# Performance work log

Measured on AMD Instinct MI355X. Metric: run time of the kernel, lower is better.

Reference implementation:

```python
import jax, jax.numpy as jnp
import numpy as np

N_FFT = 4096
HOP = 1024
WIN = 300          # wiener_win_len (frames per independent Wiener chunk)
EPS = 1e-10
SCALE_FACTOR = 10.0


def hann(n):
    # torch.hann_window (periodic)
    return 0.5 * (1.0 - jnp.cos(2.0 * jnp.pi * jnp.arange(n) / n))


def stft(x, window):
    # x: (N, C, T) -> complex (N, C, B, F), center=True, reflect pad, onesided
    pad = N_FFT // 2
    xp = jnp.pad(x, ((0, 0), (0, 0), (pad, pad)), mode='reflect')
    n_frames = 1 + (xp.shape[-1] - N_FFT) // HOP
    idx = jnp.arange(n_frames)[:, None] * HOP + jnp.arange(N_FFT)[None, :]
    frames = xp[..., idx] * window                      # (N,C,F,n_fft)
    spec = jnp.fft.rfft(frames, axis=-1)                # (N,C,F,B)
    return jnp.swapaxes(spec, -1, -2)                   # (N,C,B,F)


def istft(spec, window, length):
    # spec: (..., B, F) complex -> (..., length) real; center=True inverse
    frames = jnp.fft.irfft(jnp.swapaxes(spec, -1, -2), n=N_FFT, axis=-1) * window
    n_frames = frames.shape[-2]
    out_len = N_FFT + HOP * (n_frames - 1)
    idx = jnp.arange(n_frames)[:, None] * HOP + jnp.arange(N_FFT)[None, :]
    out = jnp.zeros(frames.shape[:-2] + (out_len,), frames.dtype).at[..., idx].add(frames)
    wsum = jnp.zeros((out_len,), frames.dtype).at[idx].add(
        jnp.broadcast_to(window ** 2, idx.shape))
    out = out / jnp.where(wsum > 1e-11, wsum, 1.0)
    pad = N_FFT // 2
    return out[..., pad:pad + length]


def wiener_chunk(v, x, niter):
    # openunmix.filtering.wiener (softmask=False, residual=False) on one chunk.
    # v: (T, B, C, S) real target magnitudes; x: (T, B, C) complex mix STFT.
    phase = jnp.exp(1j * jnp.angle(x))                  # mixture phase init
    y = (v * phase[..., None]).astype(jnp.complex64)    # (T,B,C,S)
    max_abs = jnp.maximum(1.0, jnp.max(jnp.abs(x)) / SCALE_FACTOR)
    x = x / max_abs
    y = y / max_abs
    C = x.shape[-1]
    reg = np.sqrt(EPS) * jnp.eye(C, dtype=jnp.complex64)
    for _ in range(niter):  # expectation_maximization, one pass per iter
        psd = jnp.mean(jnp.abs(y) ** 2, axis=2)         # (T,B,S) channel-avg PSD
        # spatial covariance per bin/source, normalized by eps + sum_t psd
        R = jnp.einsum('tbcs,tbds->bcds', y, jnp.conj(y))
        R = R / (EPS + jnp.sum(psd, axis=0))[:, None, None, :]
        Cxx = reg + jnp.einsum('tbs,bcds->tbcd', psd.astype(jnp.complex64), R)
        inv = jnp.linalg.inv(Cxx)                       # (T,B,C,C)
        gain = jnp.einsum('bacs,tbcd->tbads', R, inv) * psd[:, :, None, None, :]
        y = jnp.einsum('tbacs,tbc->tbas', gain, x)      # (T,B,C,S)
    return y * max_abs


def setup_inputs() -> dict:
    key = jax.random.key(0)
    k1, k2 = jax.random.split(key)
    audio = jax.random.normal(k1, (2, 2, 613376), dtype=jnp.float32)
    W = jax.random.normal(k2, (4, 2049), dtype=jnp.float32)  # per-target per-bin mask logits
    return {'audio': audio, 'W': W, 'niter': 1}


def reference(audio, W, niter):
    window = hann(N_FFT).astype(audio.dtype)
    mix = stft(audio, window)                           # (N,C,B,F) complex
    X = jnp.abs(mix)                                    # ComplexNorm power=1
    # target models (stand-in: per-bin sigmoid masks); input detached as in torch
    Xd = jax.lax.stop_gradient(X)
    masks = jax.nn.sigmoid(W)                           # (S,B)
    specs = Xd[..., None] * jnp.transpose(masks)[None, None, :, None, :]  # (N,C,B,F,S)
    v = jnp.transpose(specs, (0, 3, 2, 1, 4))           # (N,F,B,C,S)
    xm = jnp.transpose(mix, (0, 3, 2, 1))               # (N,F,B,C)
    N, F, B, C = xm.shape
    S = v.shape[-1]
    n_chunks = F // WIN
    vc = v.reshape(N, n_chunks, WIN, B, C, S)
    xc = xm.reshape(N, n_chunks, WIN, B, C)
    wfun = lambda vv, xx: wiener_chunk(vv, xx, niter)
    yc = jax.vmap(jax.vmap(wfun))(vc, xc)               # (N,chunks,T,B,C,S)
    y = yc.reshape(N, F, B, C, S)
    y = jnp.transpose(y, (0, 4, 3, 2, 1))               # (N,S,C,B,F)
    estimates = istft(y, window, audio.shape[-1])       # (N,S,C,T)
    return estimates
```

## Files before the change

### kernel.cpp

```cpp
#include <hip/hip_runtime.h>
#include <math.h>

#define TLEN 613376
#define OLEN 617472
#define NFR  600
#define NB   2049
#define PI_F  3.14159265358979323846f
#define PI2_F 6.28318530717958647693f
#define PHYS(i) ((i) + ((i) >> 4))

__device__ __forceinline__ float winf(int j) {
  return 0.5f - 0.5f * __cosf(1.5339807878856412e-3f * (float)j);
}

__device__ __forceinline__ float wsum_at(int m) {
  int f_max = m >> 10; if (f_max > 599) f_max = 599;
  int f_min = (m - 3072) >> 10; if (f_min < 0) f_min = 0;
  float ws = 0.f;
  for (int f2 = f_min; f2 <= f_max; ++f2) {
    float w = winf(m - (f2 << 10));
    ws += w * w;
  }
  return (ws > 1e-11f) ? ws : 1.0f;
}

__device__ __forceinline__ float reflect_load(const float* __restrict__ x, int pos) {
  int k = pos - 2048;
  if (k < 0) k = -k;
  else if (k >= TLEN) k = 2 * TLEN - 2 - k;
  return x[k];
}

__device__ __forceinline__ float2 cmul(float2 a, float2 b) {
  return make_float2(a.x * b.x - a.y * b.y, a.x * b.y + a.y * b.x);
}
__device__ __forceinline__ float2 cadd(float2 a, float2 b) { return make_float2(a.x + b.x, a.y + b.y); }
__device__ __forceinline__ float2 csub(float2 a, float2 b) { return make_float2(a.x - b.x, a.y - b.y); }
template<int SGN>
__device__ __forceinline__ float2 muli(float2 a) {
  return (SGN > 0) ? make_float2(-a.y, a.x) : make_float2(a.y, -a.x);
}

template<int SGN>
__device__ __forceinline__ void fft4(float2 v[4]) {
  float2 t0 = cadd(v[0], v[2]), t1 = csub(v[0], v[2]);
  float2 t2 = cadd(v[1], v[3]), t3 = csub(v[1], v[3]);
  float2 it3 = muli<SGN>(t3);
  v[0] = cadd(t0, t2); v[2] = csub(t0, t2);
  v[1] = cadd(t1, it3); v[3] = csub(t1, it3);
}

template<int SGN>
__device__ __forceinline__ void fft8(float2 v[8]) {
  const float C = 0.70710678118654752440f;
  const float s = (SGN > 0) ? 1.0f : -1.0f;
  float2 t0 = cadd(v[0], v[4]), t1 = csub(v[0], v[4]);
  float2 t2 = cadd(v[2], v[6]), t3 = csub(v[2], v[6]);
  float2 e0 = cadd(t0, t2), e2 = csub(t0, t2);
  float2 it3 = muli<SGN>(t3);
  float2 e1 = cadd(t1, it3), e3 = csub(t1, it3);
  t0 = cadd(v[1], v[5]); t1 = csub(v[1], v[5]);
  t2 = cadd(v[3], v[7]); t3 = csub(v[3], v[7]);
  float2 o0 = cadd(t0, t2), o2 = csub(t0, t2);
  it3 = muli<SGN>(t3);
  float2 o1 = cadd(t1, it3), o3 = csub(t1, it3);
  float2 o1w = make_float2(C * (o1.x - s * o1.y), C * (o1.y + s * o1.x));
  float2 o2w = muli<SGN>(o2);
  float2 o3w = make_float2(C * (-o3.x - s * o3.y), C * (-o3.y + s * o3.x));
  v[0] = cadd(e0, o0);  v[4] = csub(e0, o0);
  v[1] = cadd(e1, o1w); v[5] = csub(e1, o1w);
  v[2] = cadd(e2, o2w); v[6] = csub(e2, o2w);
  v[3] = cadd(e3, o3w); v[7] = csub(e3, o3w);
}

template<int SGN>
__device__ __forceinline__ void twiddle8(float2 v[8], float ang) {
  float sn, cs;
  __sincosf((SGN > 0) ? ang : -ang, &sn, &cs);
  float2 w1 = make_float2(cs, sn);
  float2 w = w1;
  v[1] = cmul(v[1], w);
#pragma unroll
  for (int r = 2; r < 8; ++r) { w = cmul(w, w1); v[r] = cmul(v[r], w); }
}

template<int SGN>
__device__ __forceinline__ void fft2048_mid(float2* lds, float2 v[8], int tid) {
  fft8<SGN>(v);
#pragma unroll
  for (int r = 0; r < 8; ++r) { int i = tid * 8 + r; lds[PHYS(i)] = v[r]; }
  __syncthreads();
#pragma unroll
  for (int r = 0; r < 8; ++r) v[r] = lds[PHYS(tid + 256 * r)];
  twiddle8<SGN>(v, PI2_F * (1.0f / 64.0f) * (float)(tid & 7));
  fft8<SGN>(v);
  __syncthreads();
#pragma unroll
  for (int r = 0; r < 8; ++r) { int i = ((tid >> 3) << 6) + (tid & 7) + 8 * r; lds[PHYS(i)] = v[r]; }
  __syncthreads();
#pragma unroll
  for (int r = 0; r < 8; ++r) v[r] = lds[PHYS(tid + 256 * r)];
  twiddle8<SGN>(v, PI2_F * (1.0f / 512.0f) * (float)(tid & 63));
  fft8<SGN>(v);
  __syncthreads();
#pragma unroll
  for (int r = 0; r < 8; ++r) { int i = ((tid >> 6) << 9) + (tid & 63) + 64 * r; lds[PHYS(i)] = v[r]; }
  __syncthreads();
}

template<int SGN>
__device__ __forceinline__ void fft2048_last(const float2* lds, int jj, float2 u[4]) {
#pragma unroll
  for (int r = 0; r < 4; ++r) u[r] = lds[PHYS(jj + 512 * r)];
  float sn, cs;
  float ang = PI2_F * (1.0f / 2048.0f) * (float)jj;
  __sincosf((SGN > 0) ? ang : -ang, &sn, &cs);
  float2 w1 = make_float2(cs, sn);
  float2 w2 = cmul(w1, w1);
  float2 w3 = cmul(w2, w1);
  u[1] = cmul(u[1], w1); u[2] = cmul(u[2], w2); u[3] = cmul(u[3], w3);
  fft4<SGN>(u);
}

__global__ __launch_bounds__(256, 6) void stft_kernel(const float* __restrict__ audio,
                                                      float2* __restrict__ X) {
  __shared__ float2 lds[2176];
  int bid = blockIdx.x;
  int f  = bid % NFR;
  int nc = bid / NFR;
  const float* x = audio + (size_t)nc * TLEN;
  int tid = threadIdx.x;
  int base = f * 1024;
  float2 v[8];
#pragma unroll
  for (int r = 0; r < 8; ++r) {
    int k = tid + 256 * r;
    int j0 = 2 * k;
    v[r] = make_float2(reflect_load(x, base + j0)     * winf(j0),
                       reflect_load(x, base + j0 + 1) * winf(j0 + 1));
  }
  fft2048_mid<-1>(lds, v, tid);
  fft2048_last<-1>(lds, tid,        v);
  fft2048_last<-1>(lds, tid + 256,  v + 4);
  __syncthreads();
#pragma unroll
  for (int r = 0; r < 4; ++r) lds[PHYS(tid + 512 * r)] = v[r];
#pragma unroll
  for (int r = 0; r < 4; ++r) lds[PHYS(tid + 256 + 512 * r)] = v[4 + r];
  __syncthreads();
  float2* out = X + (size_t)bid * NB;
  float sn0, cs0;
  __sincosf(-PI_F * (float)tid * (1.0f / 2048.0f), &sn0, &cs0);
  float2 ph = make_float2(cs0, sn0);
  const float2 rot = make_float2(0.92387953251128675613f, -0.38268343236508977173f);
#pragma unroll
  for (int r = 0; r < 9; ++r) {
    int k = tid + 256 * r;
    if (k <= 2048) {
      float2 Zk = lds[PHYS(k & 2047)];
      float2 Zm = lds[PHYS((2048 - k) & 2047)];
      float Ex = 0.5f * (Zk.x + Zm.x), Ey = 0.5f * (Zk.y - Zm.y);
      float Dx = 0.5f * (Zk.x - Zm.x), Dy = 0.5f * (Zk.y + Zm.y);
      float Ox = Dy, Oy = -Dx;
      out[k] = make_float2(Ex + Ox * ph.x - Oy * ph.y, Ey + Ox * ph.y + Oy * ph.x);
    }
    ph = cmul(ph, rot);
  }
}

__global__ __launch_bounds__(256) void stats_kernel(const float2* __restrict__ X,
                                                    float* __restrict__ stats4,
                                                    unsigned int* __restrict__ maxsq) {
  __shared__ unsigned int sm;
  if (threadIdx.x == 0) sm = 0u;
  __syncthreads();
  int b = blockIdx.x * 256 + threadIdx.x;
  bool ok = (b < NB);
  int g = blockIdx.y;
  int n = g >> 1, chunk = g & 1;
  int t0 = blockIdx.z * 75;
  const float2* X0 = X + ((size_t)(n * 2 + 0) * NFR + chunk * 300 + t0) * NB + (ok ? b : 0);
  const float2* X1 = X + ((size_t)(n * 2 + 1) * NFR + chunk * 300 + t0) * NB + (ok ? b : 0);
  float s00 = 0.f, s11 = 0.f, sre = 0.f, sim = 0.f, lmax = 0.f;
  if (ok) {
    for (int t = 0; t < 75; ++t) {
      float2 a = X0[(size_t)t * NB];
      float2 c = X1[(size_t)t * NB];
      float pa = a.x * a.x + a.y * a.y;
      float pc = c.x * c.x + c.y * c.y;
      s00 += pa; s11 += pc;
      sre += a.x * c.x + a.y * c.y;
      sim += a.y * c.x - a.x * c.y;
      lmax = fmaxf(lmax, fmaxf(pa, pc));
    }
  }
  atomicMax(&sm, __float_as_uint(lmax));
  __syncthreads();
  if (threadIdx.x == 0) atomicMax(&maxsq[g], sm);
  if (ok) {
    float* sp = stats4 + ((size_t)g * NB + b) * 4;
    unsafeAtomicAdd(sp + 0, s00);
    unsafeAtomicAdd(sp + 1, s11);
    unsafeAtomicAdd(sp + 2, sre);
    unsafeAtomicAdd(sp + 3, sim);
  }
}

__global__ __launch_bounds__(256) void alpha_kernel(const float* __restrict__ Wmask,
                                                    const float4* __restrict__ stats4,
                                                    const unsigned int* __restrict__ maxsq,
                                                    float* __restrict__ alpha,
                                                    float* __restrict__ Ksum) {
  int idx = blockIdx.x * 256 + threadIdx.x;
  if (idx >= 4 * NB) return;
  int b = idx % NB;
  int g = idx / NB;
  float ma2 = fmaxf(1.0f, __uint_as_float(maxsq[g]) * 0.01f);
  float4 s4 = stats4[(size_t)g * NB + b];
  float P = 0.5f * (s4.x + s4.y) / ma2;
  float K = 0.f;
#pragma unroll
  for (int s = 0; s < 4; ++s) {
    float mv = 1.0f / (1.0f + expf(-Wmask[s * NB + b]));
    float m2 = mv * mv;
    float a = (m2 * m2) / (1e-10f + m2 * P);
    alpha[(size_t)(g * 4 + s) * NB + b] = a;
    K += a;
  }
  Ksum[(size_t)g * NB + b] = K;
}

__global__ __launch_bounds__(256) void wiener_kernel(const float2* __restrict__ X,
                                                     const float4* __restrict__ stats4,
                                                     const float* __restrict__ Ksum,
                                                     const unsigned int* __restrict__ maxsq,
                                                     float2* __restrict__ Wc) {
  int idx = blockIdx.x * 256 + threadIdx.x;
  if (idx >= 4 * 300 * NB) return;
  int b = idx % NB;
  int gt = idx / NB;
  int t = gt % 300;
  int g = gt / 300;
  int n = g >> 1, chunk = g & 1;
  int f = chunk * 300 + t;
  float ima2 = 1.0f / fmaxf(1.0f, __uint_as_float(maxsq[g]) * 0.01f);
  float4 s4 = stats4[(size_t)g * NB + b];
  float g00 = s4.x * ima2, g11 = s4.y * ima2, gre = s4.z * ima2, gim = s4.w * ima2;
  float K = Ksum[(size_t)g * NB + b];
  float2 x0 = X[((size_t)(n * 2 + 0) * NFR + f) * NB + b];
  float2 x1 = X[((size_t)(n * 2 + 1) * NFR + f) * NB + b];
  float ph = 0.5f * ((x0.x * x0.x + x0.y * x0.y) + (x1.x * x1.x + x1.y * x1.y)) * ima2;
  float pk = ph * K;
  float M00 = 1e-5f + pk * g00;
  float M11 = 1e-5f + pk * g11;
  float Mre = pk * gre, Mim = pk * gim;
  float det = M00 * M11 - (Mre * Mre + Mim * Mim);
  float sc = ph / det;
  float u0x = M11 * x0.x - (Mre * x1.x - Mim * x1.y);
  float u0y = M11 * x0.y - (Mre * x1.y + Mim * x1.x);
  float u1x = M00 * x1.x - (Mre * x0.x + Mim * x0.y);
  float u1y = M00 * x1.y - (Mre * x0.y - Mim * x0.x);
  float w0x = g00 * u0x + (gre * u1x - gim * u1y);
  float w0y = g00 * u0y + (gre * u1y + gim * u1x);
  float w1x = (gre * u0x + gim * u0y) + g11 * u1x;
  float w1y = (gre * u0y - gim * u0x) + g11 * u1y;
  float2* out = Wc + ((size_t)(n * NFR + f) * 2) * NB + b;
  out[0]  = make_float2(w0x * sc, w0y * sc);
  out[NB] = make_float2(w1x * sc, w1y * sc);
}

template<int MODE>
__global__ __launch_bounds__(256, 6) void istft_pass_kernel(const float2* __restrict__ Wc,
                                                            const float* __restrict__ alpha,
                                                            float* __restrict__ accum,
                                                            float* __restrict__ out,
                                                            int pass) {
  __shared__ float2 lds[2176];
  int bid = blockIdx.x;
  int fi = bid % 150;
  int plane = bid / 150;
  int c = plane & 1;
  int s = (plane >> 1) & 3;
  int n = plane >> 3;
  int f = 4 * fi + pass;
  int g = n * 2 + (f >= 300 ? 1 : 0);
  int tid = threadIdx.x;
  const float2* Wrow = Wc + ((size_t)(n * NFR + f) * 2 + c) * NB;
  const float*  arow = alpha + (size_t)(g * 4 + s) * NB;
  float* acc = accum + (size_t)plane * OLEN + (size_t)f * 1024;

  float2 pre[8];
  if (MODE >= 1) {
#pragma unroll
    for (int half = 0; half < 2; ++half) {
#pragma unroll
      for (int r = 0; r < 4; ++r) {
        int m = tid + 256 * half + 512 * r;
        pre[half * 4 + r] = *(const float2*)&acc[2 * m];
      }
    }
  }

  float2 v[8];
  float sn0, cs0;
  __sincosf(PI_F * (float)tid * (1.0f / 2048.0f), &sn0, &cs0);
  float2 ph = make_float2(cs0, sn0);
  const float2 rot = make_float2(0.92387953251128675613f, 0.38268343236508977173f);
#pragma unroll
  for (int r = 0; r < 8; ++r) {
    int k = tid + 256 * r;
    float ak = arow[k];
    float2 sk = Wrow[k]; sk.x *= ak; sk.y *= ak;
    int rk = 2048 - k;
    float am = arow[rk];
    float2 sv = Wrow[rk]; sv.x *= am; sv.y *= am;
    float Ex = 0.5f * (sk.x + sv.x), Ey = 0.5f * (sk.y - sv.y);
    float Dx = 0.5f * (sk.x - sv.x), Dy = 0.5f * (sk.y + sv.y);
    float Ox = Dx * ph.x - Dy * ph.y, Oy = Dx * ph.y + Dy * ph.x;
    v[r] = make_float2(Ex - Oy, Ey + Ox);
    ph = cmul(ph, rot);
  }
  fft2048_mid<1>(lds, v, tid);
  float* outp = out + (size_t)plane * TLEN;
  const float scale = 1.0f / 2048.0f;
#pragma unroll
  for (int half = 0; half < 2; ++half) {
    int jj = tid + 256 * half;
    float2 u[4];
    fft2048_last<1>(lds, jj, u);
#pragma unroll
    for (int r = 0; r < 4; ++r) {
      int m = jj + 512 * r;
      int j0 = 2 * m;
      float2 val = make_float2(u[r].x * scale * winf(j0),
                               u[r].y * scale * winf(j0 + 1));
      float2* p = (float2*)&acc[j0];
      if (MODE == 0) {
        *p = val;
      } else if (MODE == 1) {
        float2 o = pre[half * 4 + r];
        val.x += o.x; val.y += o.y;
        *p = val;
      } else {
        int gm = f * 1024 + j0;
        if (gm < 615424) {
          float2 o = pre[half * 4 + r];
          val.x += o.x; val.y += o.y;
          float i0, i1;
          if (gm >= 3072 && gm + 1 < 614400) {
            i0 = 0.66666666666666667f; i1 = i0;
          } else {
            i0 = 1.0f / wsum_at(gm); i1 = 1.0f / wsum_at(gm + 1);
          }
          float2* po = (float2*)&outp[gm - 2048];
          *po = make_float2(val.x * i0, val.y * i1);
        }
      }
    }
  }
  if (MODE == 0 && fi == 149) {
    float* tail = accum + (size_t)plane * OLEN + 614400;
    for (int i = tid; i < OLEN - 614400; i += 256) tail[i] = 0.f;
  }
  if (MODE == 2 && fi == 0) {
    float* accp = accum + (size_t)plane * OLEN;
    for (int m = 2048 + tid; m < 3072; m += 256) {
      outp[m - 2048] = accp[m] / wsum_at(m);
    }
  }
}

extern "C" void kernel_launch(void* const* d_in, const int* in_sizes, int n_in,
                              void* d_out, int out_size, void* d_ws, size_t ws_size,
                              hipStream_t stream) {
  const float* audio = (const float*)d_in[0];
  const float* Wmask = (const float*)d_in[1];
  float* out = (float*)d_out;

  char* ws = (char*)d_ws;
  const size_t off_stats4 = 0;
  const size_t off_maxsq  = 131136;
  const size_t zero_span  = 131200;
  const size_t off_X      = zero_span;
  const size_t off_Wc     = off_X + 39340800;
  const size_t off_accum  = off_Wc + 39340800;
  const size_t off_alpha  = off_accum + 39518208;
  const size_t off_Ksum   = off_alpha + 131136;

  float*        stats4f = (float*)(ws + off_stats4);
  float4*       stats4  = (float4*)(ws + off_stats4);
  unsigned int* maxsq   = (unsigned int*)(ws + off_maxsq);
  float2*       X       = (float2*)(ws + off_X);
  float2*       Wc      = (float2*)(ws + off_Wc);
  float*        accum   = (float*)(ws + off_accum);
  float*        alpha   = (float*)(ws + off_alpha);
  float*        Ksum    = (float*)(ws + off_Ksum);

  hipMemsetAsync(ws, 0, zero_span, stream);

  stft_kernel<<<2400, 256, 0, stream>>>(audio, X);
  stats_kernel<<<dim3(9, 4, 4), 256, 0, stream>>>(X, stats4f, maxsq);
  alpha_kernel<<<(4 * NB + 255) / 256, 256, 0, stream>>>(Wmask, stats4, maxsq, alpha, Ksum);
  wiener_kernel<<<(4 * 300 * NB + 255) / 256, 256, 0, stream>>>(X, stats4, Ksum, maxsq, Wc);
  istft_pass_kernel<0><<<2400, 256, 0, stream>>>(Wc, alpha, accum, out, 0);
  istft_pass_kernel<1><<<2400, 256, 0, stream>>>(Wc, alpha, accum, out, 1);
  istft_pass_kernel<1><<<2400, 256, 0, stream>>>(Wc, alpha, accum, out, 2);
  istft_pass_kernel<2><<<2400, 256, 0, stream>>>(Wc, alpha, accum, out, 3);
}
```

Baseline: 199.8 us.

## Store STFT spectrum and overlap-add accumulator in half precision; vectorize interior frame loads

The mixture STFT buffer X and the iSTFT overlap-add accumulator are now stored as fp16 instead of fp32, which halves the bytes written and read by the stft, stats, wiener and istft pass kernels. Interior frames also skip the reflect-index logic and load the audio as float2 vectors. The cost is reduced precision: fp16 spectra and partial sums can lose accuracy, and large STFT magnitudes could overflow the half range.

```diff
diff --git a/kernel.cpp b/kernel.cpp
--- a/kernel.cpp
+++ b/kernel.cpp
@@ -1,4 +1,5 @@
 #include <hip/hip_runtime.h>
+#include <hip/hip_fp16.h>
 #include <math.h>
 
 #define TLEN 613376
@@ -123,7 +124,7 @@
 }
 
 __global__ __launch_bounds__(256, 6) void stft_kernel(const float* __restrict__ audio,
-                                                      float2* __restrict__ X) {
+                                                      __half2* __restrict__ X) {
   __shared__ float2 lds[2176];
   int bid = blockIdx.x;
   int f  = bid % NFR;
@@ -132,12 +133,23 @@
   int tid = threadIdx.x;
   int base = f * 1024;
   float2 v[8];
-#pragma unroll
-  for (int r = 0; r < 8; ++r) {
-    int k = tid + 256 * r;
-    int j0 = 2 * k;
-    v[r] = make_float2(reflect_load(x, base + j0)     * winf(j0),
-                       reflect_load(x, base + j0 + 1) * winf(j0 + 1));
+  if (f >= 2 && f <= 597) {
+    const float2* xv = (const float2*)(x + base - 2048);
+#pragma unroll
+    for (int r = 0; r < 8; ++r) {
+      int k = tid + 256 * r;
+      float2 t = xv[k];
+      int j0 = 2 * k;
+      v[r] = make_float2(t.x * winf(j0), t.y * winf(j0 + 1));
+    }
+  } else {
+#pragma unroll
+    for (int r = 0; r < 8; ++r) {
+      int k = tid + 256 * r;
+      int j0 = 2 * k;
+      v[r] = make_float2(reflect_load(x, base + j0)     * winf(j0),
+                         reflect_load(x, base + j0 + 1) * winf(j0 + 1));
+    }
   }
   fft2048_mid<-1>(lds, v, tid);
   fft2048_last<-1>(lds, tid,        v);
@@ -148,7 +160,7 @@
 #pragma unroll
   for (int r = 0; r < 4; ++r) lds[PHYS(tid + 256 + 512 * r)] = v[4 + r];
   __syncthreads();
-  float2* out = X + (size_t)bid * NB;
+  __half2* out = X + (size_t)bid * NB;
   float sn0, cs0;
   __sincosf(-PI_F * (float)tid * (1.0f / 2048.0f), &sn0, &cs0);
   float2 ph = make_float2(cs0, sn0);
@@ -162,13 +174,13 @@
       float Ex = 0.5f * (Zk.x + Zm.x), Ey = 0.5f * (Zk.y - Zm.y);
       float Dx = 0.5f * (Zk.x - Zm.x), Dy = 0.5f * (Zk.y + Zm.y);
       float Ox = Dy, Oy = -Dx;
-      out[k] = make_float2(Ex + Ox * ph.x - Oy * ph.y, Ey + Ox * ph.y + Oy * ph.x);
+      out[k] = __floats2half2_rn(Ex + Ox * ph.x - Oy * ph.y, Ey + Ox * ph.y + Oy * ph.x);
     }
     ph = cmul(ph, rot);
   }
 }
 
-__global__ __launch_bounds__(256) void stats_kernel(const float2* __restrict__ X,
+__global__ __launch_bounds__(256) void stats_kernel(const __half2* __restrict__ X,
                                                     float* __restrict__ stats4,
                                                     unsigned int* __restrict__ maxsq) {
   __shared__ unsigned int sm;
@@ -179,13 +191,13 @@
   int g = blockIdx.y;
   int n = g >> 1, chunk = g & 1;
   int t0 = blockIdx.z * 75;
-  const float2* X0 = X + ((size_t)(n * 2 + 0) * NFR + chunk * 300 + t0) * NB + (ok ? b : 0);
-  const float2* X1 = X + ((size_t)(n * 2 + 1) * NFR + chunk * 300 + t0) * NB + (ok ? b : 0);
+  const __half2* X0 = X + ((size_t)(n * 2 + 0) * NFR + chunk * 300 + t0) * NB + (ok ? b : 0);
+  const __half2* X1 = X + ((size_t)(n * 2 + 1) * NFR + chunk * 300 + t0) * NB + (ok ? b : 0);
   float s00 = 0.f, s11 = 0.f, sre = 0.f, sim = 0.f, lmax = 0.f;
   if (ok) {
     for (int t = 0; t < 75; ++t) {
-      float2 a = X0[(size_t)t * NB];
-      float2 c = X1[(size_t)t * NB];
+      float2 a = __half22float2(X0[(size_t)t * NB]);
+      float2 c = __half22float2(X1[(size_t)t * NB]);
       float pa = a.x * a.x + a.y * a.y;
       float pc = c.x * c.x + c.y * c.y;
       s00 += pa; s11 += pc;
@@ -230,7 +242,7 @@
   Ksum[(size_t)g * NB + b] = K;
 }
 
-__global__ __launch_bounds__(256) void wiener_kernel(const float2* __restrict__ X,
+__global__ __launch_bounds__(256) void wiener_kernel(const __half2* __restrict__ X,
                                                      const float4* __restrict__ stats4,
                                                      const float* __restrict__ Ksum,
                                                      const unsigned int* __restrict__ maxsq,
@@ -247,8 +259,8 @@
   float4 s4 = stats4[(size_t)g * NB + b];
   float g00 = s4.x * ima2, g11 = s4.y * ima2, gre = s4.z * ima2, gim = s4.w * ima2;
   float K = Ksum[(size_t)g * NB + b];
-  float2 x0 = X[((size_t)(n * 2 + 0) * NFR + f) * NB + b];
-  float2 x1 = X[((size_t)(n * 2 + 1) * NFR + f) * NB + b];
+  float2 x0 = __half22float2(X[((size_t)(n * 2 + 0) * NFR + f) * NB + b]);
+  float2 x1 = __half22float2(X[((size_t)(n * 2 + 1) * NFR + f) * NB + b]);
   float ph = 0.5f * ((x0.x * x0.x + x0.y * x0.y) + (x1.x * x1.x + x1.y * x1.y)) * ima2;
   float pk = ph * K;
   float M00 = 1e-5f + pk * g00;
@@ -272,7 +284,7 @@
 template<int MODE>
 __global__ __launch_bounds__(256, 6) void istft_pass_kernel(const float2* __restrict__ Wc,
                                                             const float* __restrict__ alpha,
-                                                            float* __restrict__ accum,
+                                                            __half* __restrict__ accum,
                                                             float* __restrict__ out,
                                                             int pass) {
   __shared__ float2 lds[2176];
@@ -287,16 +299,16 @@
   int tid = threadIdx.x;
   const float2* Wrow = Wc + ((size_t)(n * NFR + f) * 2 + c) * NB;
   const float*  arow = alpha + (size_t)(g * 4 + s) * NB;
-  float* acc = accum + (size_t)plane * OLEN + (size_t)f * 1024;
-
-  float2 pre[8];
+  __half2* acc2 = (__half2*)(accum + (size_t)plane * OLEN + (size_t)f * 1024);
+
+  __half2 pre[8];
   if (MODE >= 1) {
 #pragma unroll
     for (int half = 0; half < 2; ++half) {
 #pragma unroll
       for (int r = 0; r < 4; ++r) {
         int m = tid + 256 * half + 512 * r;
-        pre[half * 4 + r] = *(const float2*)&acc[2 * m];
+        pre[half * 4 + r] = acc2[m];
       }
     }
   }
@@ -334,17 +346,15 @@
       int j0 = 2 * m;
       float2 val = make_float2(u[r].x * scale * winf(j0),
                                u[r].y * scale * winf(j0 + 1));
-      float2* p = (float2*)&acc[j0];
       if (MODE == 0) {
-        *p = val;
+        acc2[m] = __floats2half2_rn(val.x, val.y);
       } else if (MODE == 1) {
-        float2 o = pre[half * 4 + r];
-        val.x += o.x; val.y += o.y;
-        *p = val;
+        float2 o = __half22float2(pre[half * 4 + r]);
+        acc2[m] = __floats2half2_rn(val.x + o.x, val.y + o.y);
       } else {
         int gm = f * 1024 + j0;
         if (gm < 615424) {
-          float2 o = pre[half * 4 + r];
+          float2 o = __half22float2(pre[half * 4 + r]);
           val.x += o.x; val.y += o.y;
           float i0, i1;
           if (gm >= 3072 && gm + 1 < 614400) {
@@ -359,13 +369,13 @@
     }
   }
   if (MODE == 0 && fi == 149) {
-    float* tail = accum + (size_t)plane * OLEN + 614400;
-    for (int i = tid; i < OLEN - 614400; i += 256) tail[i] = 0.f;
+    __half2* tail = (__half2*)(accum + (size_t)plane * OLEN + 614400);
+    for (int i = tid; i < 1536; i += 256) tail[i] = __floats2half2_rn(0.f, 0.f);
   }
   if (MODE == 2 && fi == 0) {
-    float* accp = accum + (size_t)plane * OLEN;
+    const __half* accp = accum + (size_t)plane * OLEN;
     for (int m = 2048 + tid; m < 3072; m += 256) {
-      outp[m - 2048] = accp[m] / wsum_at(m);
+      outp[m - 2048] = __half2float(accp[m]) / wsum_at(m);
     }
   }
 }
@@ -382,17 +392,17 @@
   const size_t off_maxsq  = 131136;
   const size_t zero_span  = 131200;
   const size_t off_X      = zero_span;
-  const size_t off_Wc     = off_X + 39340800;
+  const size_t off_Wc     = off_X + 19670400;
   const size_t off_accum  = off_Wc + 39340800;
-  const size_t off_alpha  = off_accum + 39518208;
+  const size_t off_alpha  = off_accum + 19759104;
   const size_t off_Ksum   = off_alpha + 131136;
 
   float*        stats4f = (float*)(ws + off_stats4);
   float4*       stats4  = (float4*)(ws + off_stats4);
   unsigned int* maxsq   = (unsigned int*)(ws + off_maxsq);
-  float2*       X       = (float2*)(ws + off_X);
+  __half2*      X       = (__half2*)(ws + off_X);
   float2*       Wc      = (float2*)(ws + off_Wc);
-  float*        accum   = (float*)(ws + off_accum);
+  __half*       accum   = (__half*)(ws + off_accum);
   float*        alpha   = (float*)(ws + off_alpha);
   float*        Ksum    = (float*)(ws + off_Ksum);
 
```

After: 205.2 us. 1.03x slower.
